# Kernel tuning notes

Measured on AMD Instinct MI355X. Metric: run time of the kernel, lower is better.

## Reference

```python
import jax, jax.numpy as jnp
import numpy as np

N_SKILL = 50000
B = 4096          # number of (job, resume) pairs; n_job == n_resume required by the concat
E = 65536         # edges per relation (avg degree 16)
D = 1536          # embedding_dim
HID = [512, 256, 64]


def setup_inputs() -> dict:
    key = jax.random.key(0)
    ks = jax.random.split(key, 16)
    nrm = lambda k, shape, s=0.02: jax.random.normal(k, shape, dtype=jnp.float32) * s
    inp = {
        "x_skill": jax.random.normal(ks[0], (N_SKILL, D), dtype=jnp.float32),
        "x_job": jax.random.normal(ks[1], (B, D), dtype=jnp.float32),
        "x_resume": jax.random.normal(ks[2], (B, D), dtype=jnp.float32),
        "src_sj": jax.random.randint(ks[3], (E,), 0, N_SKILL),
        "dst_sj": jax.random.randint(ks[4], (E,), 0, B),
        "src_sr": jax.random.randint(ks[5], (E,), 0, N_SKILL),
        "dst_sr": jax.random.randint(ks[6], (E,), 0, B),
        "W_rel_j": nrm(ks[7], (D, D)),
        "b_rel_j": jnp.zeros((D,), jnp.float32),
        "W_root_j": nrm(ks[8], (D, D)),
        "W_rel_r": nrm(ks[9], (D, D)),
        "b_rel_r": jnp.zeros((D,), jnp.float32),
        "W_root_r": nrm(ks[10], (D, D)),
        "W1": nrm(ks[11], (2 * D, HID[0])), "b1": jnp.zeros((HID[0],), jnp.float32),
        "W2": nrm(ks[12], (HID[0], HID[1])), "b2": jnp.zeros((HID[1],), jnp.float32),
        "W3": nrm(ks[13], (HID[1], HID[2])), "b3": jnp.zeros((HID[2],), jnp.float32),
        "W4": nrm(ks[14], (HID[2], 1)), "b4": jnp.zeros((1,), jnp.float32),
    }
    return inp


def _graph_conv(x_src, x_dst, src, dst, W_rel, b_rel, W_root):
    # PyG GraphConv (aggr='add', bipartite): out = lin_rel(sum_{j in N(i)} x_j) + lin_root(x_i)
    agg = jax.ops.segment_sum(x_src[src], dst, num_segments=x_dst.shape[0])  # [B, D]
    return agg @ W_rel + b_rel + x_dst @ W_root


def reference(x_skill, x_job, x_resume, src_sj, dst_sj, src_sr, dst_sr,
              W_rel_j, b_rel_j, W_root_j, W_rel_r, b_rel_r, W_root_r,
              W1, b1, W2, b2, W3, b3, W4, b4):
    # HeteroConv: each dst node type ('job', 'resume') receives exactly one relation,
    # so the cross-relation 'mean' aggregation is the identity.
    h_job = jax.nn.relu(_graph_conv(x_skill, x_job, src_sj, dst_sj, W_rel_j, b_rel_j, W_root_j))
    h_res = jax.nn.relu(_graph_conv(x_skill, x_resume, src_sr, dst_sr, W_rel_r, b_rel_r, W_root_r))
    h = jnp.concatenate([h_job, h_res], axis=1)  # [B, 2D]
    # MLP (dropout is inference-mode identity)
    h = jax.nn.relu(h @ W1 + b1)
    h = jax.nn.relu(h @ W2 + b2)
    h = jax.nn.relu(h @ W3 + b3)
    score = (h @ W4 + b4).squeeze(-1)  # [B]
    return score
```

## Files before the change

kernel.cpp:

```cpp
#include <hip/hip_runtime.h>

#define E_EDGES 65536
#define NB 4096
#define DD 1536
#define CAP 96

typedef unsigned short u16;
typedef __bf16 bf16x8 __attribute__((ext_vector_type(8)));
typedef float f32x4 __attribute__((ext_vector_type(4)));

#define AS1(p) ((const __attribute__((address_space(1))) void*)(p))
#define AS3(p) ((__attribute__((address_space(3))) void*)(p))

#define BAR() do { __builtin_amdgcn_s_barrier(); asm volatile("" ::: "memory"); } while (0)
#define VMCNT0() asm volatile("s_waitcnt vmcnt(0)" ::: "memory")

__device__ __forceinline__ u16 f2bf(float f) {
    unsigned u = __float_as_uint(f);
    u += 0x7fffu + ((u >> 16) & 1u);
    return (u16)(u >> 16);
}


__global__ __launch_bounds__(256) void bucket_kernel(
    const int* __restrict__ sj, const int* __restrict__ dj,
    const int* __restrict__ sr, const int* __restrict__ dr,
    int* __restrict__ cnt, int* __restrict__ bkt) {
    int e = blockIdx.x * 256 + threadIdx.x;
    int rel = blockIdx.y;
    int s = rel ? sr[e] : sj[e];
    int d = rel ? dr[e] : dj[e];
    int slot = rel * NB + d;
    int pos = atomicAdd(&cnt[slot], 1);
    if (pos < CAP) bkt[(size_t)slot * CAP + pos] = s;
}


__global__ __launch_bounds__(128) void agg_cvt_kernel(
    const float* __restrict__ xskill, const float* __restrict__ xj, const float* __restrict__ xr,
    const int* __restrict__ bkt, const int* __restrict__ cnt,
    u16* __restrict__ Aj, u16* __restrict__ Ar) {
    int rel = blockIdx.y;
    int row = blockIdx.x;
    int t = threadIdx.x;
    const float* xd = (rel ? xr : xj) + (size_t)row * DD;
    u16* A = (rel ? Ar : Aj) + (size_t)row * (2 * DD);

    float4 v[3];
#pragma unroll
    for (int c = 0; c < 3; ++c) v[c] = *(const float4*)(xd + t * 4 + c * 512);
#pragma unroll
    for (int c = 0; c < 3; ++c) {
        ushort4 o = {f2bf(v[c].x), f2bf(v[c].y), f2bf(v[c].z), f2bf(v[c].w)};
        *(ushort4*)(A + DD + t * 4 + c * 512) = o;
    }

    int count = cnt[rel * NB + row];
    if (count > CAP) count = CAP;
    __shared__ int sidx[CAP];
    if (t < count) sidx[t] = bkt[(size_t)(rel * NB + row) * CAP + t];
    __syncthreads();

    float4 acc[3] = {};
    for (int e = 0; e < count; ++e) {
        const float* xs = xskill + (size_t)sidx[e] * DD;
#pragma unroll
        for (int c = 0; c < 3; ++c) {
            float4 u = *(const float4*)(xs + t * 4 + c * 512);
            acc[c].x += u.x; acc[c].y += u.y; acc[c].z += u.z; acc[c].w += u.w;
        }
    }
#pragma unroll
    for (int c = 0; c < 3; ++c) {
        ushort4 o = {f2bf(acc[c].x), f2bf(acc[c].y), f2bf(acc[c].z), f2bf(acc[c].w)};
        *(ushort4*)(A + t * 4 + c * 512) = o;
    }
}


__global__ __launch_bounds__(256) void transpose_all(
    const float* __restrict__ w0, const float* __restrict__ w1,
    const float* __restrict__ w2, const float* __restrict__ w3,
    const float* __restrict__ w4, const float* __restrict__ w5,
    u16* __restrict__ Wjt, u16* __restrict__ Wrt,
    u16* __restrict__ W1t, u16* __restrict__ W2t) {
    int bid = blockIdx.x;
    const float* in; u16* out; int N, ldo, k0, nbx;
    if (bid < 9216) {
        int m = bid / 2304;
        bid = bid % 2304;
        in = (m == 0) ? w0 : (m == 1) ? w1 : (m == 2) ? w2 : w3;
        out = (m < 2) ? Wjt : Wrt;
        N = 1536; ldo = 3072; k0 = (m & 1) ? DD : 0; nbx = 48;
    } else if (bid < 10752) {
        bid -= 9216;
        in = w4; out = W1t; N = 512; ldo = 3072; k0 = 0; nbx = 16;
    } else {
        bid -= 10752;
        in = w5; out = W2t; N = 256; ldo = 512; k0 = 0; nbx = 8;
    }
    int bx = (bid % nbx) * 32;
    int by = (bid / nbx) * 32;
    __shared__ float tile[32][33];
    int tx = threadIdx.x & 31, ty = threadIdx.x >> 5;
#pragma unroll
    for (int i = 0; i < 4; ++i)
        tile[ty + i * 8][tx] = in[(size_t)(by + ty + i * 8) * N + bx + tx];
    __syncthreads();
#pragma unroll
    for (int i = 0; i < 4; ++i) {
        int n = bx + ty + i * 8;
        int k = by + tx;
        out[(size_t)n * ldo + k0 + k] = f2bf(tile[tx][ty + i * 8]);
    }
}


__global__ __launch_bounds__(512, 2) void conv_gemm256(
    const u16* __restrict__ Aj, const u16* __restrict__ Wjt, const float* __restrict__ bj,
    const u16* __restrict__ Ar, const u16* __restrict__ Wrt, const float* __restrict__ br,
    u16* __restrict__ C) {
    constexpr int K = 3072, NT = K / 64, LDC = 3072;
    __shared__ u16 lds[65536];
    int tid = threadIdx.x;
    int lane = tid & 63;
    int w = tid >> 6;

    int bid = blockIdx.y * 16 + blockIdx.x;
    bid = (bid & 7) * 12 + (bid >> 3);
    long bm = (long)(bid % 16) * 256;
    long bn = (long)(bid / 16) * 256;

    const u16* A; const u16* Bt; const float* bias; long cofs;
    if (blockIdx.z) { A = Ar; Bt = Wrt; bias = br; cofs = DD; }
    else            { A = Aj; Bt = Wjt; bias = bj; cofs = 0;  }

    int wm = (w >> 2) * 128;
    int wn = (w & 3) * 64;

    const int sr0 = (w * 2) * 8 + (lane >> 3);
    const int sr1 = (w * 2 + 1) * 8 + (lane >> 3);
    const int skf = ((lane & 7) * 8) ^ ((lane >> 3) << 3);

    auto stageA = [&](int b, int h, long k0) {
        const u16* g0 = A + (bm + h * 128 + sr0) * (long)K + k0 + skf;
        const u16* g1 = A + (bm + h * 128 + sr1) * (long)K + k0 + skf;
        __builtin_amdgcn_global_load_lds(AS1(g0), AS3(lds + b * 32768 + h * 8192 + (w * 2 + 0) * 512), 16, 0, 0);
        __builtin_amdgcn_global_load_lds(AS1(g1), AS3(lds + b * 32768 + h * 8192 + (w * 2 + 1) * 512), 16, 0, 0);
    };
    auto stageB = [&](int b, int h, long k0) {
        const u16* g0 = Bt + (bn + h * 128 + sr0) * (long)K + k0 + skf;
        const u16* g1 = Bt + (bn + h * 128 + sr1) * (long)K + k0 + skf;
        __builtin_amdgcn_global_load_lds(AS1(g0), AS3(lds + b * 32768 + 16384 + h * 8192 + (w * 2 + 0) * 512), 16, 0, 0);
        __builtin_amdgcn_global_load_lds(AS1(g1), AS3(lds + b * 32768 + 16384 + h * 8192 + (w * 2 + 1) * 512), 16, 0, 0);
    };

    const int lrow = lane & 15;
    const int lko = (lane >> 4) * 8;
    const int rsw = (lane & 7) << 3;

    auto ldA = [&](int b, int mi, int kk) -> bf16x8 {
        return *(const bf16x8*)(lds + b * 32768 + (wm + mi * 16 + lrow) * 64 + ((kk + lko) ^ rsw));
    };
    auto ldB = [&](int b, int nj, int kk) -> bf16x8 {
        return *(const bf16x8*)(lds + b * 32768 + 16384 + (wn + nj * 16 + lrow) * 64 + ((kk + lko) ^ rsw));
    };

    f32x4 acc[8][4] = {};

    stageA(0, 0, 0); stageA(0, 1, 0);
    stageB(0, 0, 0); stageB(0, 1, 0);

    for (int t = 0; t < NT; ++t) {
        int b = t & 1;
        VMCNT0();
        BAR();
        if (t + 1 < NT) {
            long k1 = (long)(t + 1) * 64;
            stageA(b ^ 1, 0, k1); stageA(b ^ 1, 1, k1);
            stageB(b ^ 1, 0, k1); stageB(b ^ 1, 1, k1);
        }
#pragma unroll
        for (int kk = 0; kk < 64; kk += 32) {
            bf16x8 bfr[4];
#pragma unroll
            for (int nj = 0; nj < 4; ++nj) bfr[nj] = ldB(b, nj, kk);
#pragma unroll
            for (int h = 0; h < 2; ++h) {
                bf16x8 af[4];
#pragma unroll
                for (int mi = 0; mi < 4; ++mi) af[mi] = ldA(b, h * 4 + mi, kk);
                __builtin_amdgcn_s_setprio(1);
#pragma unroll
                for (int mi = 0; mi < 4; ++mi)
#pragma unroll
                    for (int nj = 0; nj < 4; ++nj)
                        acc[h * 4 + mi][nj] = __builtin_amdgcn_mfma_f32_16x16x32_bf16(af[mi], bfr[nj], acc[h * 4 + mi][nj], 0, 0, 0);
                __builtin_amdgcn_s_setprio(0);
            }
        }
    }

    int rb = (lane >> 4) * 4, cl = lane & 15;
#pragma unroll
    for (int mi = 0; mi < 8; ++mi)
#pragma unroll
        for (int nj = 0; nj < 4; ++nj) {
            long row = bm + wm + mi * 16 + rb;
            long col = bn + wn + nj * 16 + cl;
            float bb = bias[col];
#pragma unroll
            for (int r = 0; r < 4; ++r) {
                float v = fmaxf(acc[mi][nj][r] + bb, 0.f);
                C[(row + r) * (long)LDC + cofs + col] = f2bf(v);
            }
        }
}


template <int BM, bool OUT_BF16>
__global__ __launch_bounds__(256, 2) void gemm_bias_relu(
    const u16* __restrict__ A, const u16* __restrict__ Bt, const float* __restrict__ bias,
    void* __restrict__ C, int K, int ldc) {
    constexpr int BK = 64;
    constexpr int MI = BM / 32;
    constexpr int NITER = (BM + 128) / 32;
    constexpr int TILE = (BM + 128) * BK;
    __shared__ u16 lds[2 * TILE];
    int tid = threadIdx.x;
    int lane = tid & 63;
    int w = tid >> 6;
    long bm = (long)blockIdx.x * BM;
    long bn = (long)blockIdx.y * 128;
    int wm = (w >> 1) * (BM / 2), wn = (w & 1) * 64;
    f32x4 acc[MI][4] = {};
    const int lrow = lane & 15;
    const int lko = (lane >> 4) * 8;

    auto stage = [&](int buf, long k0) {
#pragma unroll
        for (int i = 0; i < NITER; ++i) {
            int chunk = i * 256 + tid;
            int row = chunk >> 3, kc = chunk & 7;
            if (row < BM) {
                const u16* g = A + (bm + row) * (long)K + k0 + kc * 8;
                __builtin_amdgcn_global_load_lds(AS1(g), AS3((char*)(lds + (size_t)buf * TILE) + i * 4096 + w * 1024), 16, 0, 0);
            } else {
                const u16* g = Bt + (bn + row - BM) * (long)K + k0 + kc * 8;
                __builtin_amdgcn_global_load_lds(AS1(g), AS3((char*)(lds + (size_t)buf * TILE) + i * 4096 + w * 1024), 16, 0, 0);
            }
        }
    };

    stage(0, 0);
    const int nt = K / BK;
    for (int t = 0; t < nt; ++t) {
        int b = t & 1;
        VMCNT0();
        BAR();
        if (t + 1 < nt) stage(b ^ 1, (long)(t + 1) * BK);
        const u16* lA = lds + (size_t)b * TILE;
        const u16* lB = lA + BM * BK;
#pragma unroll
        for (int kk = 0; kk < BK; kk += 32) {
            bf16x8 af[MI], bfr[4];
#pragma unroll
            for (int i = 0; i < MI; ++i)
                af[i] = *(const bf16x8*)(lA + (wm + i * 16 + lrow) * BK + kk + lko);
#pragma unroll
            for (int j = 0; j < 4; ++j)
                bfr[j] = *(const bf16x8*)(lB + (wn + j * 16 + lrow) * BK + kk + lko);
            __builtin_amdgcn_s_setprio(1);
#pragma unroll
            for (int i = 0; i < MI; ++i)
#pragma unroll
                for (int j = 0; j < 4; ++j)
                    acc[i][j] = __builtin_amdgcn_mfma_f32_16x16x32_bf16(af[i], bfr[j], acc[i][j], 0, 0, 0);
            __builtin_amdgcn_s_setprio(0);
        }
    }

    int rb = (lane >> 4) * 4, cl = lane & 15;
#pragma unroll
    for (int i = 0; i < MI; ++i)
#pragma unroll
        for (int j = 0; j < 4; ++j) {
            long row = bm + wm + i * 16 + rb;
            long col = bn + wn + j * 16 + cl;
            float b = bias[col];
#pragma unroll
            for (int r = 0; r < 4; ++r) {
                float v = fmaxf(acc[i][j][r] + b, 0.f);
                long o = (row + r) * (long)ldc + col;
                if (OUT_BF16)
                    ((u16*)C)[o] = f2bf(v);
                else
                    ((float*)C)[o] = v;
            }
        }
}


__global__ __launch_bounds__(64) void l34_kernel(
    const float* __restrict__ h2, const float* __restrict__ W3, const float* __restrict__ b3,
    const float* __restrict__ W4, const float* __restrict__ b4, float* __restrict__ out) {
    int t = threadIdx.x;
    __shared__ float hrow[256];
    float w4t = W4[t];
    float b3t = b3[t];
    for (int rr = 0; rr < 16; ++rr) {
        int row = blockIdx.x * 16 + rr;
        __syncthreads();
        ((float4*)hrow)[t] = ((const float4*)(h2 + (size_t)row * 256))[t];
        __syncthreads();
        float acc = b3t;
#pragma unroll 8
        for (int k = 0; k < 256; ++k) acc = fmaf(hrow[k], W3[k * 64 + t], acc);
        acc = fmaxf(acc, 0.f);
        float s = acc * w4t;
#pragma unroll
        for (int o = 32; o > 0; o >>= 1) s += __shfl_down(s, o);
        if (t == 0) out[row] = s + b4[0];
    }
}


extern "C" void kernel_launch(void* const* d_in, const int* in_sizes, int n_in,
                              void* d_out, int out_size, void* d_ws, size_t ws_size,
                              hipStream_t stream) {
    (void)in_sizes; (void)n_in; (void)out_size; (void)ws_size;
    const float* x_skill  = (const float*)d_in[0];
    const float* x_job    = (const float*)d_in[1];
    const float* x_resume = (const float*)d_in[2];
    const int* src_sj = (const int*)d_in[3];
    const int* dst_sj = (const int*)d_in[4];
    const int* src_sr = (const int*)d_in[5];
    const int* dst_sr = (const int*)d_in[6];
    const float* W_rel_j  = (const float*)d_in[7];
    const float* b_rel_j  = (const float*)d_in[8];
    const float* W_root_j = (const float*)d_in[9];
    const float* W_rel_r  = (const float*)d_in[10];
    const float* b_rel_r  = (const float*)d_in[11];
    const float* W_root_r = (const float*)d_in[12];
    const float* W1 = (const float*)d_in[13];
    const float* b1 = (const float*)d_in[14];
    const float* W2 = (const float*)d_in[15];
    const float* b2 = (const float*)d_in[16];
    const float* W3 = (const float*)d_in[17];
    const float* b3 = (const float*)d_in[18];
    const float* W4 = (const float*)d_in[19];
    const float* b4 = (const float*)d_in[20];
    float* out = (float*)d_out;

    char* p = (char*)d_ws;
    auto alloc = [&](size_t bytes) -> char* {
        char* r = p;
        p += (bytes + 255) & ~(size_t)255;
        return r;
    };
    int* cnt = (int*)alloc(2 * NB * 4);
    int* bkt = (int*)alloc((size_t)2 * NB * CAP * 4);
    u16* Aj   = (u16*)alloc((size_t)NB * 2 * DD * 2);
    u16* Ar   = (u16*)alloc((size_t)NB * 2 * DD * 2);
    u16* Wjt  = (u16*)alloc((size_t)DD * 2 * DD * 2);
    u16* Wrt  = (u16*)alloc((size_t)DD * 2 * DD * 2);
    u16* W1t  = (u16*)alloc((size_t)512 * 3072 * 2);
    u16* W2t  = (u16*)alloc((size_t)256 * 512 * 2);
    u16* hcat = (u16*)alloc((size_t)NB * 3072 * 2);
    u16* h1   = (u16*)alloc((size_t)NB * 512 * 2);
    float* h2 = (float*)alloc((size_t)NB * 256 * 4);

    hipMemsetAsync(cnt, 0, 2 * NB * 4, stream);
    bucket_kernel<<<dim3(E_EDGES / 256, 2), 256, 0, stream>>>(src_sj, dst_sj, src_sr, dst_sr, cnt, bkt);
    transpose_all<<<10880, 256, 0, stream>>>(W_rel_j, W_root_j, W_rel_r, W_root_r, W1, W2,
                                             Wjt, Wrt, W1t, W2t);
    agg_cvt_kernel<<<dim3(NB, 2), 128, 0, stream>>>(x_skill, x_job, x_resume, bkt, cnt, Aj, Ar);

    conv_gemm256<<<dim3(16, 6, 2), 512, 0, stream>>>(Aj, Wjt, b_rel_j, Ar, Wrt, b_rel_r, hcat);
    gemm_bias_relu<64, true><<<dim3(NB / 64, 512 / 128), 256, 0, stream>>>(hcat, W1t, b1, h1, 3072, 512);
    gemm_bias_relu<64, false><<<dim3(NB / 64, 256 / 128), 256, 0, stream>>>(h1, W2t, b2, h2, 512, 256);
    l34_kernel<<<NB / 16, 64, 0, stream>>>(h2, W3, b3, W4, b4, out);
}
```

Baseline: 380.7 us.

## Retile conv GEMM to 256x192, fuse bucketing into prep, simplify MLP GEMM

```diff
diff --git a/kernel.cpp b/kernel.cpp
--- a/kernel.cpp
+++ b/kernel.cpp
@@ -22,69 +22,27 @@
 }
 
 
-__global__ __launch_bounds__(256) void bucket_kernel(
-    const int* __restrict__ sj, const int* __restrict__ dj,
-    const int* __restrict__ sr, const int* __restrict__ dr,
-    int* __restrict__ cnt, int* __restrict__ bkt) {
-    int e = blockIdx.x * 256 + threadIdx.x;
-    int rel = blockIdx.y;
-    int s = rel ? sr[e] : sj[e];
-    int d = rel ? dr[e] : dj[e];
-    int slot = rel * NB + d;
-    int pos = atomicAdd(&cnt[slot], 1);
-    if (pos < CAP) bkt[(size_t)slot * CAP + pos] = s;
-}
-
-
-__global__ __launch_bounds__(128) void agg_cvt_kernel(
-    const float* __restrict__ xskill, const float* __restrict__ xj, const float* __restrict__ xr,
-    const int* __restrict__ bkt, const int* __restrict__ cnt,
-    u16* __restrict__ Aj, u16* __restrict__ Ar) {
-    int rel = blockIdx.y;
-    int row = blockIdx.x;
-    int t = threadIdx.x;
-    const float* xd = (rel ? xr : xj) + (size_t)row * DD;
-    u16* A = (rel ? Ar : Aj) + (size_t)row * (2 * DD);
-
-    float4 v[3];
-#pragma unroll
-    for (int c = 0; c < 3; ++c) v[c] = *(const float4*)(xd + t * 4 + c * 512);
-#pragma unroll
-    for (int c = 0; c < 3; ++c) {
-        ushort4 o = {f2bf(v[c].x), f2bf(v[c].y), f2bf(v[c].z), f2bf(v[c].w)};
-        *(ushort4*)(A + DD + t * 4 + c * 512) = o;
-    }
-
-    int count = cnt[rel * NB + row];
-    if (count > CAP) count = CAP;
-    __shared__ int sidx[CAP];
-    if (t < count) sidx[t] = bkt[(size_t)(rel * NB + row) * CAP + t];
-    __syncthreads();
-
-    float4 acc[3] = {};
-    for (int e = 0; e < count; ++e) {
-        const float* xs = xskill + (size_t)sidx[e] * DD;
-#pragma unroll
-        for (int c = 0; c < 3; ++c) {
-            float4 u = *(const float4*)(xs + t * 4 + c * 512);
-            acc[c].x += u.x; acc[c].y += u.y; acc[c].z += u.z; acc[c].w += u.w;
-        }
-    }
-#pragma unroll
-    for (int c = 0; c < 3; ++c) {
-        ushort4 o = {f2bf(acc[c].x), f2bf(acc[c].y), f2bf(acc[c].z), f2bf(acc[c].w)};
-        *(ushort4*)(A + t * 4 + c * 512) = o;
-    }
-}
-
-
-__global__ __launch_bounds__(256) void transpose_all(
+__global__ __launch_bounds__(256) void prep_kernel(
     const float* __restrict__ w0, const float* __restrict__ w1,
     const float* __restrict__ w2, const float* __restrict__ w3,
     const float* __restrict__ w4, const float* __restrict__ w5,
     u16* __restrict__ Wjt, u16* __restrict__ Wrt,
-    u16* __restrict__ W1t, u16* __restrict__ W2t) {
+    u16* __restrict__ W1t, u16* __restrict__ W2t,
+    const int* __restrict__ sj, const int* __restrict__ dj,
+    const int* __restrict__ sr, const int* __restrict__ dr,
+    int* __restrict__ cnt, int* __restrict__ bkt) {
     int bid = blockIdx.x;
+    if (bid >= 10880) {
+        int b2 = bid - 10880;
+        int rel = b2 >> 8;
+        int e = (b2 & 255) * 256 + threadIdx.x;
+        int s = rel ? sr[e] : sj[e];
+        int d = rel ? dr[e] : dj[e];
+        int slot = rel * NB + d;
+        int pos = atomicAdd(&cnt[slot], 1);
+        if (pos < CAP) bkt[(size_t)slot * CAP + pos] = s;
+        return;
+    }
     const float* in; u16* out; int N, ldo, k0, nbx;
     if (bid < 9216) {
         int m = bid / 2304;
@@ -116,43 +74,89 @@
 }
 
 
-__global__ __launch_bounds__(512, 2) void conv_gemm256(
+__global__ __launch_bounds__(128) void agg_cvt_kernel(
+    const float* __restrict__ xskill, const float* __restrict__ xj, const float* __restrict__ xr,
+    const int* __restrict__ bkt, const int* __restrict__ cnt,
+    u16* __restrict__ Aj, u16* __restrict__ Ar) {
+    int rel = blockIdx.y;
+    int row = blockIdx.x;
+    int t = threadIdx.x;
+    const float* xd = (rel ? xr : xj) + (size_t)row * DD;
+    u16* A = (rel ? Ar : Aj) + (size_t)row * (2 * DD);
+
+    float4 v[3];
+#pragma unroll
+    for (int c = 0; c < 3; ++c) v[c] = *(const float4*)(xd + t * 4 + c * 512);
+#pragma unroll
+    for (int c = 0; c < 3; ++c) {
+        ushort4 o = {f2bf(v[c].x), f2bf(v[c].y), f2bf(v[c].z), f2bf(v[c].w)};
+        *(ushort4*)(A + DD + t * 4 + c * 512) = o;
+    }
+
+    int count = cnt[rel * NB + row];
+    if (count > CAP) count = CAP;
+    __shared__ int sidx[CAP];
+    if (t < count) sidx[t] = bkt[(size_t)(rel * NB + row) * CAP + t];
+    __syncthreads();
+
+    float4 acc[3] = {};
+    for (int e = 0; e < count; ++e) {
+        const float* xs = xskill + (size_t)sidx[e] * DD;
+#pragma unroll
+        for (int c = 0; c < 3; ++c) {
+            float4 u = *(const float4*)(xs + t * 4 + c * 512);
+            acc[c].x += u.x; acc[c].y += u.y; acc[c].z += u.z; acc[c].w += u.w;
+        }
+    }
+#pragma unroll
+    for (int c = 0; c < 3; ++c) {
+        ushort4 o = {f2bf(acc[c].x), f2bf(acc[c].y), f2bf(acc[c].z), f2bf(acc[c].w)};
+        *(ushort4*)(A + t * 4 + c * 512) = o;
+    }
+}
+
+
+__global__ __launch_bounds__(512, 2) void conv_gemm(
     const u16* __restrict__ Aj, const u16* __restrict__ Wjt, const float* __restrict__ bj,
     const u16* __restrict__ Ar, const u16* __restrict__ Wrt, const float* __restrict__ br,
     u16* __restrict__ C) {
     constexpr int K = 3072, NT = K / 64, LDC = 3072;
-    __shared__ u16 lds[65536];
+    constexpr int BUF = 28672;
+    __shared__ u16 lds[2 * BUF];
     int tid = threadIdx.x;
     int lane = tid & 63;
     int w = tid >> 6;
 
-    int bid = blockIdx.y * 16 + blockIdx.x;
-    bid = (bid & 7) * 12 + (bid >> 3);
-    long bm = (long)(bid % 16) * 256;
-    long bn = (long)(bid / 16) * 256;
+    int p = blockIdx.y * 16 + blockIdx.x;
+    int lg = (p & 7) * 16 + (p >> 3);
+    long bm = (long)(lg & 15) * 256;
+    long bn = (long)(lg >> 4) * 192;
 
     const u16* A; const u16* Bt; const float* bias; long cofs;
     if (blockIdx.z) { A = Ar; Bt = Wrt; bias = br; cofs = DD; }
     else            { A = Aj; Bt = Wjt; bias = bj; cofs = 0;  }
 
     int wm = (w >> 2) * 128;
-    int wn = (w & 3) * 64;
-
-    const int sr0 = (w * 2) * 8 + (lane >> 3);
-    const int sr1 = (w * 2 + 1) * 8 + (lane >> 3);
+    int wn = (w & 3) * 48;
+
+    const int srow = lane >> 3;
     const int skf = ((lane & 7) * 8) ^ ((lane >> 3) << 3);
 
-    auto stageA = [&](int b, int h, long k0) {
-        const u16* g0 = A + (bm + h * 128 + sr0) * (long)K + k0 + skf;
-        const u16* g1 = A + (bm + h * 128 + sr1) * (long)K + k0 + skf;
-        __builtin_amdgcn_global_load_lds(AS1(g0), AS3(lds + b * 32768 + h * 8192 + (w * 2 + 0) * 512), 16, 0, 0);
-        __builtin_amdgcn_global_load_lds(AS1(g1), AS3(lds + b * 32768 + h * 8192 + (w * 2 + 1) * 512), 16, 0, 0);
-    };
-    auto stageB = [&](int b, int h, long k0) {
-        const u16* g0 = Bt + (bn + h * 128 + sr0) * (long)K + k0 + skf;
-        const u16* g1 = Bt + (bn + h * 128 + sr1) * (long)K + k0 + skf;
-        __builtin_amdgcn_global_load_lds(AS1(g0), AS3(lds + b * 32768 + 16384 + h * 8192 + (w * 2 + 0) * 512), 16, 0, 0);
-        __builtin_amdgcn_global_load_lds(AS1(g1), AS3(lds + b * 32768 + 16384 + h * 8192 + (w * 2 + 1) * 512), 16, 0, 0);
+    auto stageA = [&](int b, long k0) {
+#pragma unroll
+        for (int i = 0; i < 4; ++i) {
+            int g = i * 8 + w;
+            const u16* gp = A + (bm + g * 8 + srow) * (long)K + k0 + skf;
+            __builtin_amdgcn_global_load_lds(AS1(gp), AS3(lds + b * BUF + g * 512), 16, 0, 0);
+        }
+    };
+    auto stageB = [&](int b, long k0) {
+#pragma unroll
+        for (int i = 0; i < 3; ++i) {
+            int g = i * 8 + w;
+            const u16* gp = Bt + (bn + g * 8 + srow) * (long)K + k0 + skf;
+            __builtin_amdgcn_global_load_lds(AS1(gp), AS3(lds + b * BUF + 16384 + g * 512), 16, 0, 0);
+        }
     };
 
     const int lrow = lane & 15;
@@ -160,16 +164,15 @@
     const int rsw = (lane & 7) << 3;
 
     auto ldA = [&](int b, int mi, int kk) -> bf16x8 {
-        return *(const bf16x8*)(lds + b * 32768 + (wm + mi * 16 + lrow) * 64 + ((kk + lko) ^ rsw));
+        return *(const bf16x8*)(lds + b * BUF + (wm + mi * 16 + lrow) * 64 + ((kk + lko) ^ rsw));
     };
     auto ldB = [&](int b, int nj, int kk) -> bf16x8 {
-        return *(const bf16x8*)(lds + b * 32768 + 16384 + (wn + nj * 16 + lrow) * 64 + ((kk + lko) ^ rsw));
-    };
-
-    f32x4 acc[8][4] = {};
-
-    stageA(0, 0, 0); stageA(0, 1, 0);
-    stageB(0, 0, 0); stageB(0, 1, 0);
+        return *(const bf16x8*)(lds + b * BUF + 16384 + (wn + nj * 16 + lrow) * 64 + ((kk + lko) ^ rsw));
+    };
+
+    f32x4 acc[8][3] = {};
+
+    stageA(0, 0); stageB(0, 0);
 
     for (int t = 0; t < NT; ++t) {
         int b = t & 1;
@@ -177,14 +180,13 @@
         BAR();
         if (t + 1 < NT) {
             long k1 = (long)(t + 1) * 64;
-            stageA(b ^ 1, 0, k1); stageA(b ^ 1, 1, k1);
-            stageB(b ^ 1, 0, k1); stageB(b ^ 1, 1, k1);
+            stageA(b ^ 1, k1); stageB(b ^ 1, k1);
         }
 #pragma unroll
         for (int kk = 0; kk < 64; kk += 32) {
-            bf16x8 bfr[4];
-#pragma unroll
-            for (int nj = 0; nj < 4; ++nj) bfr[nj] = ldB(b, nj, kk);
+            bf16x8 bfr[3];
+#pragma unroll
+            for (int nj = 0; nj < 3; ++nj) bfr[nj] = ldB(b, nj, kk);
 #pragma unroll
             for (int h = 0; h < 2; ++h) {
                 bf16x8 af[4];
@@ -194,7 +196,7 @@
 #pragma unroll
                 for (int mi = 0; mi < 4; ++mi)
 #pragma unroll
-                    for (int nj = 0; nj < 4; ++nj)
+                    for (int nj = 0; nj < 3; ++nj)
                         acc[h * 4 + mi][nj] = __builtin_amdgcn_mfma_f32_16x16x32_bf16(af[mi], bfr[nj], acc[h * 4 + mi][nj], 0, 0, 0);
                 __builtin_amdgcn_s_setprio(0);
             }
@@ -205,7 +207,7 @@
 #pragma unroll
     for (int mi = 0; mi < 8; ++mi)
 #pragma unroll
-        for (int nj = 0; nj < 4; ++nj) {
+        for (int nj = 0; nj < 3; ++nj) {
             long row = bm + wm + mi * 16 + rb;
             long col = bn + wn + nj * 16 + cl;
             float bb = bias[col];
@@ -219,14 +221,14 @@
 
 
 template <int BM, bool OUT_BF16>
-__global__ __launch_bounds__(256, 2) void gemm_bias_relu(
+__global__ __launch_bounds__(256) void gemm_bias_relu(
     const u16* __restrict__ A, const u16* __restrict__ Bt, const float* __restrict__ bias,
     void* __restrict__ C, int K, int ldc) {
     constexpr int BK = 64;
     constexpr int MI = BM / 32;
     constexpr int NITER = (BM + 128) / 32;
-    constexpr int TILE = (BM + 128) * BK;
-    __shared__ u16 lds[2 * TILE];
+    __shared__ u16 lA[BM * BK];
+    __shared__ u16 lB[128 * BK];
     int tid = threadIdx.x;
     int lane = tid & 63;
     int w = tid >> 6;
@@ -237,30 +239,20 @@
     const int lrow = lane & 15;
     const int lko = (lane >> 4) * 8;
 
-    auto stage = [&](int buf, long k0) {
+    for (int k0 = 0; k0 < K; k0 += BK) {
 #pragma unroll
         for (int i = 0; i < NITER; ++i) {
             int chunk = i * 256 + tid;
             int row = chunk >> 3, kc = chunk & 7;
             if (row < BM) {
                 const u16* g = A + (bm + row) * (long)K + k0 + kc * 8;
-                __builtin_amdgcn_global_load_lds(AS1(g), AS3((char*)(lds + (size_t)buf * TILE) + i * 4096 + w * 1024), 16, 0, 0);
+                __builtin_amdgcn_global_load_lds(AS1(g), AS3((char*)lA + i * 4096 + w * 1024), 16, 0, 0);
             } else {
                 const u16* g = Bt + (bn + row - BM) * (long)K + k0 + kc * 8;
-                __builtin_amdgcn_global_load_lds(AS1(g), AS3((char*)(lds + (size_t)buf * TILE) + i * 4096 + w * 1024), 16, 0, 0);
+                __builtin_amdgcn_global_load_lds(AS1(g), AS3((char*)lB + i * 4096 + w * 1024 - BM * 128), 16, 0, 0);
             }
         }
-    };
-
-    stage(0, 0);
-    const int nt = K / BK;
-    for (int t = 0; t < nt; ++t) {
-        int b = t & 1;
-        VMCNT0();
-        BAR();
-        if (t + 1 < nt) stage(b ^ 1, (long)(t + 1) * BK);
-        const u16* lA = lds + (size_t)b * TILE;
-        const u16* lB = lA + BM * BK;
+        __syncthreads();
 #pragma unroll
         for (int kk = 0; kk < BK; kk += 32) {
             bf16x8 af[MI], bfr[4];
@@ -270,14 +262,13 @@
 #pragma unroll
             for (int j = 0; j < 4; ++j)
                 bfr[j] = *(const bf16x8*)(lB + (wn + j * 16 + lrow) * BK + kk + lko);
-            __builtin_amdgcn_s_setprio(1);
 #pragma unroll
             for (int i = 0; i < MI; ++i)
 #pragma unroll
                 for (int j = 0; j < 4; ++j)
                     acc[i][j] = __builtin_amdgcn_mfma_f32_16x16x32_bf16(af[i], bfr[j], acc[i][j], 0, 0, 0);
-            __builtin_amdgcn_s_setprio(0);
-        }
+        }
+        __syncthreads();
     }
 
     int rb = (lane >> 4) * 4, cl = lane & 15;
@@ -308,8 +299,8 @@
     __shared__ float hrow[256];
     float w4t = W4[t];
     float b3t = b3[t];
-    for (int rr = 0; rr < 16; ++rr) {
-        int row = blockIdx.x * 16 + rr;
+    for (int rr = 0; rr < 4; ++rr) {
+        int row = blockIdx.x * 4 + rr;
         __syncthreads();
         ((float4*)hrow)[t] = ((const float4*)(h2 + (size_t)row * 256))[t];
         __syncthreads();
@@ -371,13 +362,13 @@
     float* h2 = (float*)alloc((size_t)NB * 256 * 4);
 
     hipMemsetAsync(cnt, 0, 2 * NB * 4, stream);
-    bucket_kernel<<<dim3(E_EDGES / 256, 2), 256, 0, stream>>>(src_sj, dst_sj, src_sr, dst_sr, cnt, bkt);
-    transpose_all<<<10880, 256, 0, stream>>>(W_rel_j, W_root_j, W_rel_r, W_root_r, W1, W2,
-                                             Wjt, Wrt, W1t, W2t);
+    prep_kernel<<<11392, 256, 0, stream>>>(W_rel_j, W_root_j, W_rel_r, W_root_r, W1, W2,
+                                           Wjt, Wrt, W1t, W2t,
+                                           src_sj, dst_sj, src_sr, dst_sr, cnt, bkt);
     agg_cvt_kernel<<<dim3(NB, 2), 128, 0, stream>>>(x_skill, x_job, x_resume, bkt, cnt, Aj, Ar);
 
-    conv_gemm256<<<dim3(16, 6, 2), 512, 0, stream>>>(Aj, Wjt, b_rel_j, Ar, Wrt, b_rel_r, hcat);
+    conv_gemm<<<dim3(16, 8, 2), 512, 0, stream>>>(Aj, Wjt, b_rel_j, Ar, Wrt, b_rel_r, hcat);
     gemm_bias_relu<64, true><<<dim3(NB / 64, 512 / 128), 256, 0, stream>>>(hcat, W1t, b1, h1, 3072, 512);
     gemm_bias_relu<64, false><<<dim3(NB / 64, 256 / 128), 256, 0, stream>>>(h1, W2t, b2, h2, 512, 256);
-    l34_kernel<<<NB / 16, 64, 0, stream>>>(h2, W3, b3, W4, b4, out);
-}
+    l34_kernel<<<NB / 4, 64, 0, stream>>>(h2, W3, b3, W4, b4, out);
+}
```

Result: faster. 340.5 us (-10.6%).
